# Optimization experiments

Measured on AMD Instinct MI355X. Metric: run time of the kernel, lower is better.

Reference implementation:

```python
import jax, jax.numpy as jnp
import numpy as np

B, C, H, W = 2, 128, 64, 256
G, P, EXP = 8, 4, 2
D = C // G


def _conv1x1(x, w, b):
    # x: (b,c,h,w), w: (o,c), b: (o,)
    return jnp.einsum('bchw,oc->bohw', x, w) + b[None, :, None, None]


def _lin_sample(value, x):
    # value: (b,g,d,h,w); x: (b,g,p,h,w) pixel coords along W -> (b,g,d,p,h,w)
    Bv, Gv, Dv, Hv, Wv = value.shape
    Pv = x.shape[2]
    xc = jnp.clip(x, 0.0, Wv - 1.0)
    x0 = jnp.floor(xc)
    i0 = x0.astype(jnp.int32)
    i1 = jnp.minimum(i0 + 1, Wv - 1)
    t = (xc - x0)[:, :, None]  # (b,g,1,p,h,w)
    shape = (Bv, Gv, Dv, Pv, Hv, Wv)
    v = jnp.broadcast_to(value[:, :, :, None], shape)
    v0 = jnp.take_along_axis(v, jnp.broadcast_to(i0[:, :, None], shape), axis=-1)
    v1 = jnp.take_along_axis(v, jnp.broadcast_to(i1[:, :, None], shape), axis=-1)
    return v0 * (1.0 - t) + v1 * t


def _layernorm_c(x, g, b):
    mu = jnp.mean(x, axis=1, keepdims=True)
    var = jnp.mean((x - mu) ** 2, axis=1, keepdims=True)
    return (x - mu) * jax.lax.rsqrt(var + 1e-5) * g[None, :, None, None] + b[None, :, None, None]


def _forward(ml, mr, fl, fr, nl, nr, gml, gmr, cap, gap,
             wv, bv, wn, bn, woc, boc, wog, bog, wa, ba, wo, bo,
             lw, lb, w1, b1, w2, b2):
    mask = jnp.concatenate([gml, gmr], axis=0)   # (2B,1,H,W)
    q = jnp.concatenate([ml, mr], axis=0)        # (2B,C,H,W)
    ctx = jnp.concatenate([fr, fl], axis=0)      # cross: right feats for left queries
    geo = jnp.concatenate([nr, nl], axis=0)      # (2B,3,H,W)
    B2 = q.shape[0]
    # deformable 1D cross-attention (normal-guided)
    value = _conv1x1(ctx, wv, bv).reshape(B2, G, D, H, W)
    nfeat = _conv1x1(geo, wn, bn).reshape(B2, G, D, H, W)
    off_c = _conv1x1(q, woc, boc).reshape(B2, G, P, H, W)
    off_g = _conv1x1(q, wog, bog).reshape(B2, G, P, H, W)
    attn = jax.nn.softmax(_conv1x1(q, wa, ba).reshape(B2, G, 2 * P, H, W), axis=2)
    ctx_kp = jnp.clip(cap * (W - 1.0) + off_c, 0.0, W - 1.0)
    geo_kp = jnp.clip(gap * (W - 1.0) + off_g, 0.0, W - 1.0)
    s_ctx = _lin_sample(value, ctx_kp)           # (2B,G,D,P,H,W)
    s_geo = _lin_sample(nfeat, geo_kp)
    sampled = jnp.concatenate([s_ctx, s_geo], axis=3)  # (2B,G,D,2P,H,W)
    agg = jnp.einsum('bgdphw,bgphw->bgdhw', sampled, attn).reshape(B2, C, H, W)
    upd = _conv1x1(agg, wo, bo) * mask
    # residual + LayerNorm over channels + 1x1-conv FFN
    x = q + upd
    x = _layernorm_c(x, lw, lb)
    h1 = _conv1x1(x, w1, b1)
    x = x + _conv1x1(h1 * jax.nn.sigmoid(h1), w2, b2)
    return x, ctx_kp, geo_kp


def setup_inputs() -> dict:
    key = jax.random.key(0)
    ks = jax.random.split(key, 20)
    f32 = jnp.float32
    def n(k, shape, s=1.0):
        return jax.random.normal(k, shape, dtype=f32) * s
    return {
        'match_left': n(ks[0], (B, C, H, W)),
        'match_right': n(ks[1], (B, C, H, W)),
        'feat_left': n(ks[2], (B, C, H, W)),
        'feat_right': n(ks[3], (B, C, H, W)),
        'normal_left': n(ks[4], (B, 3, H, W)),
        'normal_right': n(ks[5], (B, 3, H, W)),
        'gate_mask_left': jax.random.uniform(ks[6], (B, 1, H, W), dtype=f32),
        'gate_mask_right': jax.random.uniform(ks[7], (B, 1, H, W), dtype=f32),
        'context_anchor_points': jax.random.uniform(ks[8], (2 * B, G, P, H, W), dtype=f32),
        'geometric_anchor_points': jax.random.uniform(ks[9], (2 * B, G, P, H, W), dtype=f32),
        'w_value': n(ks[10], (C, C), 0.02), 'b_value': jnp.zeros((C,), f32),
        'w_normal': n(ks[11], (C, 3), 0.02), 'b_normal': jnp.zeros((C,), f32),
        'w_off_ctx': n(ks[12], (G * P, C), 0.02), 'b_off_ctx': jnp.zeros((G * P,), f32),
        'w_off_geo': n(ks[13], (G * P, C), 0.02), 'b_off_geo': jnp.zeros((G * P,), f32),
        'w_attn': n(ks[14], (G * 2 * P, C), 0.02), 'b_attn': jnp.zeros((G * 2 * P,), f32),
        'w_out': n(ks[15], (C, C), 0.02), 'b_out': jnp.zeros((C,), f32),
        'ln_w': jnp.ones((C,), f32), 'ln_b': jnp.zeros((C,), f32),
        'w_ff1': n(ks[16], (EXP * C, C), 0.02), 'b_ff1': jnp.zeros((EXP * C,), f32),
        'w_ff2': n(ks[17], (C, EXP * C), 0.02), 'b_ff2': jnp.zeros((C,), f32),
    }


def reference(match_left, match_right, feat_left, feat_right, normal_left, normal_right,
              gate_mask_left, gate_mask_right, context_anchor_points, geometric_anchor_points,
              w_value, b_value, w_normal, b_normal, w_off_ctx, b_off_ctx, w_off_geo, b_off_geo,
              w_attn, b_attn, w_out, b_out, ln_w, ln_b, w_ff1, b_ff1, w_ff2, b_ff2):
    x, ckp, gkp = _forward(match_left, match_right, feat_left, feat_right, normal_left, normal_right,
                           gate_mask_left, gate_mask_right, context_anchor_points, geometric_anchor_points,
                           w_value, b_value, w_normal, b_normal, w_off_ctx, b_off_ctx, w_off_geo, b_off_geo,
                           w_attn, b_attn, w_out, b_out, ln_w, ln_b, w_ff1, b_ff1, w_ff2, b_ff2)
    ml, mr = jnp.split(x, 2, axis=0)
    return (ml, mr, ckp, gkp)
```

## Files before the change

### kernel.cpp

```cpp
#include <hip/hip_runtime.h>
#include <cstdint>
#include <math.h>

#define B2v 4
#define Cc  128
#define Hh  64
#define Ww  256
#define Gg  8
#define Pp  4
#define HW  (Hh*Ww)
#define CHW (Cc*HW)
#define PIT 136

typedef float f32x4 __attribute__((ext_vector_type(4)));
typedef float f32x2 __attribute__((ext_vector_type(2)));
typedef short s16x8 __attribute__((ext_vector_type(8)));
typedef short s16x4 __attribute__((ext_vector_type(4)));

__device__ __forceinline__ short f2bf(float x) {
    union { float f; unsigned u; } a; a.f = x;
    unsigned r = a.u + 0x7fffu + ((a.u >> 16) & 1u);
    return (short)(r >> 16);
}
__device__ __forceinline__ float bf2f(short s) {
    union { unsigned u; float f; } a; a.u = ((unsigned)(unsigned short)s) << 16;
    return a.f;
}
__device__ __forceinline__ unsigned cvtpk(float lo, float hi) {
    unsigned r;
    asm("v_cvt_pk_bf16_f32 %0, %1, %2" : "=v"(r) : "v"(lo), "v"(hi));
    return r;
}
__device__ __forceinline__ f32x2 unpk(unsigned w) {
    union { unsigned u; float f; } lo, hi;
    lo.u = w << 16; hi.u = w & 0xffff0000u;
    return (f32x2){lo.f, hi.f};
}
__device__ __forceinline__ float frcp(float x) { return __builtin_amdgcn_rcpf(x); }
__device__ __forceinline__ float fexp(float x) { return __expf(x); }

__global__ __launch_bounds__(256) void prep_kernel(
    const float* __restrict__ wv, const float* __restrict__ woc,
    const float* __restrict__ wog, const float* __restrict__ wa,
    const float* __restrict__ wo, const float* __restrict__ w1,
    const float* __restrict__ w2,
    const float* __restrict__ boc, const float* __restrict__ bog,
    const float* __restrict__ ba,
    short* __restrict__ wbf, float* __restrict__ bq)
{
    int i = blockIdx.x * 256 + threadIdx.x;
    if (i < 16384) wbf[i] = f2bf(wv[i]);
    else if (i < 32768) {
        int j = i - 16384; int r = j >> 7, c = j & 127;
        float v = (r < 32) ? woc[r * 128 + c] : (r < 64) ? wog[(r - 32) * 128 + c]
                                              : wa[(r - 64) * 128 + c];
        wbf[i] = f2bf(v);
    }
    else if (i < 49152)  wbf[i] = f2bf(wo[i - 32768]);
    else if (i < 81920)  wbf[i] = f2bf(w1[i - 49152]);
    else if (i < 114688) wbf[i] = f2bf(w2[i - 81920]);
    else if (i < 114816) {
        int r = i - 114688;
        bq[r] = (r < 32) ? boc[r] : (r < 64) ? bog[r - 32] : ba[r - 64];
    }
}

__global__ __launch_bounds__(1024, 4) void mega_kernel(
    const float* __restrict__ mlq, const float* __restrict__ mrq,
    const float* __restrict__ fl,  const float* __restrict__ fr,
    const float* __restrict__ nl,  const float* __restrict__ nr,
    const float* __restrict__ gml, const float* __restrict__ gmr,
    const float* __restrict__ cap, const float* __restrict__ gap,
    const short* __restrict__ wbf, const float* __restrict__ bq,
    const float* __restrict__ bv,
    const float* __restrict__ wn,  const float* __restrict__ bn,
    const float* __restrict__ bo,
    const float* __restrict__ lnw, const float* __restrict__ lnb,
    const float* __restrict__ b1,  const float* __restrict__ b2,
    float* __restrict__ out_ml, float* __restrict__ out_mr,
    float* __restrict__ ckp_out, float* __restrict__ gkp_out)
{
    __shared__ short buf1[256 * PIT];
    __shared__ short buf2[256 * PIT];
    __shared__ f32x4 sgeo4[256];
    __shared__ f32x2 swnp[256];
    __shared__ float sln[256];
    __shared__ float redS[1024], redQ[1024];
    __shared__ float smu[256], srs[256];

    const short* wv_bf = wbf;
    const short* wq_bf = wbf + 16384;
    const short* wo_bf = wbf + 32768;
    const short* w1_bf = wbf + 49152;
    const short* w2_bf = wbf + 81920;

    const int t    = threadIdx.x;
    const int lane = t & 63;
    const int wvid = t >> 6;
    const int rw   = wvid & 7;
    const int pw   = wvid >> 3;
    const int lm   = lane & 15;
    const int lq   = lane >> 4;
    const int h = blockIdx.x, b = blockIdx.y;
    const int hWw = h * Ww;
    const int px   = t & 255;
    const int qt   = t >> 8;

    const float* ctx = (b < 2) ? fr + (size_t)b * CHW : fl + (size_t)(b - 2) * CHW;
    const float* q   = (b < 2) ? mlq + (size_t)b * CHW : mrq + (size_t)(b - 2) * CHW;
    const float* geo = (b < 2) ? nr + (size_t)b * 3 * HW : nl + (size_t)(b - 2) * 3 * HW;
    const float* msk = (b < 2) ? gml + (size_t)b * HW : gmr + (size_t)(b - 2) * HW;
    float* outp = (b < 2) ? out_ml + (size_t)b * CHW : out_mr + (size_t)(b - 2) * CHW;

    float capr[8], gapr[8];
    const size_t kbase = ((size_t)b * Gg + qt * 2) * Pp * (size_t)HW + hWw + px;
    {
#pragma unroll
        for (int i = 0; i < 8; i++) {
            capr[i] = cap[kbase + (size_t)i * HW];
            gapr[i] = gap[kbase + (size_t)i * HW];
        }
    }

    if (t < 256) {
        sgeo4[t] = (f32x4){geo[hWw + t], geo[HW + hWw + t], geo[2 * HW + hWw + t], 0.f};
        const int pr = t >> 2, m = t & 3;
        const int ch0 = pr * 2, ch1 = ch0 + 1;
        float a0 = (m < 3) ? wn[ch0 * 3 + m] : bn[ch0];
        float a1 = (m < 3) ? wn[ch1 * 3 + m] : bn[ch1];
        swnp[t] = (f32x2){a0, a1};
    }
    else if (t < 512) {
        int i = t - 256;
        sln[i] = (i < 128) ? lnw[i] : lnb[i - 128];
    }

    {
        const int c0 = wvid * 8;
        const int p0 = lane * 4;
        const size_t gbase = (size_t)c0 * HW + hWw + p0;
        {
            f32x4 L[8];
#pragma unroll
            for (int c = 0; c < 8; c++) L[c] = *(const f32x4*)(ctx + gbase + (size_t)c * HW);
#pragma unroll
            for (int j = 0; j < 4; j++) {
                uint4 w0;
                w0.x = cvtpk(L[0][j], L[1][j]);  w0.y = cvtpk(L[2][j], L[3][j]);
                w0.z = cvtpk(L[4][j], L[5][j]);  w0.w = cvtpk(L[6][j], L[7][j]);
                *(uint4*)(&buf1[(p0 + j) * PIT + c0]) = w0;
            }
        }
        {
            f32x4 L[8];
#pragma unroll
            for (int c = 0; c < 8; c++) L[c] = *(const f32x4*)(q + gbase + (size_t)c * HW);
#pragma unroll
            for (int j = 0; j < 4; j++) {
                uint4 w0;
                w0.x = cvtpk(L[0][j], L[1][j]);  w0.y = cvtpk(L[2][j], L[3][j]);
                w0.z = cvtpk(L[4][j], L[5][j]);  w0.w = cvtpk(L[6][j], L[7][j]);
                *(uint4*)(&buf2[(p0 + j) * PIT + c0]) = w0;
            }
        }
    }
    __syncthreads();

    f32x4 accv[8];
#pragma unroll
    for (int nt = 0; nt < 8; nt++) accv[nt] = (f32x4){0.f, 0.f, 0.f, 0.f};
#pragma unroll
    for (int kk = 0; kk < 4; kk++) {
        s16x8 a = *(const s16x8*)(wv_bf + (size_t)(rw * 16 + lm) * 128 + kk * 32 + lq * 8);
#pragma unroll
        for (int nt = 0; nt < 8; nt++) {
            s16x8 bfv = *(const s16x8*)(&buf1[((pw * 8 + nt) * 16 + lm) * PIT + kk * 32 + lq * 8]);
            accv[nt] = __builtin_amdgcn_mfma_f32_16x16x32_bf16(a, bfv, accv[nt], 0, 0, 0);
        }
    }
    __syncthreads();

    {
        const int ob = rw * 16 + lq * 4;
        float bias[4];
#pragma unroll
        for (int r = 0; r < 4; r++) bias[r] = bv[ob + r];
#pragma unroll
        for (int nt = 0; nt < 8; nt++) {
            const int wg = (pw * 8 + nt) * 16 + lm;
            uint2 pk;
            pk.x = cvtpk(accv[nt][0] + bias[0], accv[nt][1] + bias[1]);
            pk.y = cvtpk(accv[nt][2] + bias[2], accv[nt][3] + bias[3]);
            *(uint2*)(&buf1[wg * PIT + ob]) = pk;
        }
    }
    f32x4 accp[8];
#pragma unroll
    for (int nt = 0; nt < 8; nt++) accp[nt] = (f32x4){0.f, 0.f, 0.f, 0.f};
#pragma unroll
    for (int kk = 0; kk < 4; kk++) {
        s16x8 a = *(const s16x8*)(wq_bf + (size_t)(rw * 16 + lm) * 128 + kk * 32 + lq * 8);
#pragma unroll
        for (int nt = 0; nt < 8; nt++) {
            s16x8 bfv = *(const s16x8*)(&buf2[((pw * 8 + nt) * 16 + lm) * PIT + kk * 32 + lq * 8]);
            accp[nt] = __builtin_amdgcn_mfma_f32_16x16x32_bf16(a, bfv, accp[nt], 0, 0, 0);
        }
    }
    __syncthreads();

    {
        const int ob = rw * 16 + lq * 4;
        float bias[4];
#pragma unroll
        for (int r = 0; r < 4; r++) bias[r] = bq[ob + r];
#pragma unroll
        for (int nt = 0; nt < 8; nt++) {
            const int wg = (pw * 8 + nt) * 16 + lm;
            uint2 pk;
            pk.x = cvtpk(accp[nt][0] + bias[0], accp[nt][1] + bias[1]);
            pk.y = cvtpk(accp[nt][2] + bias[2], accp[nt][3] + bias[3]);
            *(uint2*)(&buf2[wg * PIT + ob]) = pk;
        }
    }
    __syncthreads();

    float attnr[2][8], kpr[2][8];
#pragma unroll
    for (int gi = 0; gi < 2; gi++) {
        const int g = qt * 2 + gi;
        s16x8 lg = *(const s16x8*)(&buf2[px * PIT + 64 + g * 8]);
        float L[8], m = -1e30f;
#pragma unroll
        for (int j = 0; j < 8; j++) { L[j] = bf2f(lg[j]); m = fmaxf(m, L[j]); }
        float s = 0.f;
#pragma unroll
        for (int j = 0; j < 8; j++) { L[j] = fexp(L[j] - m); s += L[j]; }
        float inv = frcp(s);
#pragma unroll
        for (int j = 0; j < 8; j++) attnr[gi][j] = L[j] * inv;
#pragma unroll
        for (int p = 0; p < 4; p++) {
            size_t kidx = kbase + (size_t)(gi * 4 + p) * HW;
            float oc = bf2f(buf2[px * PIT + g * 4 + p]);
            float og = bf2f(buf2[px * PIT + 32 + g * 4 + p]);
            float ck = fminf(fmaxf(capr[gi * 4 + p] * 255.0f + oc, 0.f), 255.f);
            float gk = fminf(fmaxf(gapr[gi * 4 + p] * 255.0f + og, 0.f), 255.f);
            ckp_out[kidx] = ck;
            gkp_out[kidx] = gk;
            kpr[gi][p] = ck;
            kpr[gi][4 + p] = gk;
        }
    }
    __syncthreads();

#pragma unroll
    for (int gi = 0; gi < 2; gi++) {
        const int g = qt * 2 + gi;
        f32x2 A[8];
#pragma unroll
        for (int k = 0; k < 8; k++) A[k] = (f32x2){0.f, 0.f};
#pragma unroll
        for (int j = 0; j < 4; j++) {
            float x = kpr[gi][j];
            float fx = floorf(x);
            int i0 = (int)fx;
            int i1 = min(i0 + 1, Ww - 1);
            float tt = x - fx;
            float c0 = attnr[gi][j] * (1.f - tt);
            float c1 = attnr[gi][j] * tt;
            f32x2 c0v = {c0, c0}, c1v = {c1, c1};
            uint4 v0a = *(const uint4*)(&buf1[i0 * PIT + g * 16]);
            uint4 v0b = *(const uint4*)(&buf1[i0 * PIT + g * 16 + 8]);
            uint4 v1a = *(const uint4*)(&buf1[i1 * PIT + g * 16]);
            uint4 v1b = *(const uint4*)(&buf1[i1 * PIT + g * 16 + 8]);
            const unsigned w0[8] = {v0a.x, v0a.y, v0a.z, v0a.w, v0b.x, v0b.y, v0b.z, v0b.w};
            const unsigned w1[8] = {v1a.x, v1a.y, v1a.z, v1a.w, v1b.x, v1b.y, v1b.z, v1b.w};
#pragma unroll
            for (int k = 0; k < 8; k++)
                A[k] += unpk(w0[k]) * c0v + unpk(w1[k]) * c1v;
        }
        {
            float gs0 = 0.f, gs1 = 0.f, gs2 = 0.f, as = 0.f;
#pragma unroll
            for (int j = 4; j < 8; j++) {
                float x = kpr[gi][j];
                float fx = floorf(x);
                int i0 = (int)fx;
                int i1 = min(i0 + 1, Ww - 1);
                float tt = x - fx;
                float c0 = attnr[gi][j] * (1.f - tt);
                float c1 = attnr[gi][j] * tt;
                f32x4 ga = sgeo4[i0], gb = sgeo4[i1];
                gs0 += c0 * ga[0] + c1 * gb[0];
                gs1 += c0 * ga[1] + c1 * gb[1];
                gs2 += c0 * ga[2] + c1 * gb[2];
                as  += attnr[gi][j];
            }
            f32x2 g0v = {gs0, gs0}, g1v = {gs1, gs1}, g2v = {gs2, gs2}, asv = {as, as};
#pragma unroll
            for (int k = 0; k < 8; k++) {
                const f32x2* wp = &swnp[(g * 8 + k) * 4];
                A[k] += wp[0] * g0v + wp[1] * g1v + wp[2] * g2v + wp[3] * asv;
            }
        }
        uint4 o0, o1;
        o0.x = cvtpk(A[0][0], A[0][1]); o0.y = cvtpk(A[1][0], A[1][1]);
        o0.z = cvtpk(A[2][0], A[2][1]); o0.w = cvtpk(A[3][0], A[3][1]);
        o1.x = cvtpk(A[4][0], A[4][1]); o1.y = cvtpk(A[5][0], A[5][1]);
        o1.z = cvtpk(A[6][0], A[6][1]); o1.w = cvtpk(A[7][0], A[7][1]);
        *(uint4*)(&buf2[px * PIT + g * 16])     = o0;
        *(uint4*)(&buf2[px * PIT + g * 16 + 8]) = o1;
    }
    __syncthreads();

    {
        f32x4 acc1[8];
#pragma unroll
        for (int nt = 0; nt < 8; nt++) acc1[nt] = (f32x4){0.f, 0.f, 0.f, 0.f};
#pragma unroll
        for (int kk = 0; kk < 4; kk++) {
            s16x8 a = *(const s16x8*)(wo_bf + (size_t)(rw * 16 + lm) * 128 + kk * 32 + lq * 8);
#pragma unroll
            for (int nt = 0; nt < 8; nt++) {
                s16x8 bfv = *(const s16x8*)(&buf2[((pw * 8 + nt) * 16 + lm) * PIT + kk * 32 + lq * 8]);
                acc1[nt] = __builtin_amdgcn_mfma_f32_16x16x32_bf16(a, bfv, acc1[nt], 0, 0, 0);
            }
        }
        const int ob = rw * 16 + lq * 4;
        float bias[4];
#pragma unroll
        for (int r = 0; r < 4; r++) bias[r] = bo[ob + r];
#pragma unroll
        for (int nt = 0; nt < 8; nt++) {
            const int wg = (pw * 8 + nt) * 16 + lm;
            float mval = msk[hWw + wg];
            float xv[4];
#pragma unroll
            for (int r = 0; r < 4; r++) {
                float upd = acc1[nt][r] + bias[r];
                float qv = q[(size_t)(ob + r) * HW + hWw + wg];
                xv[r] = qv + upd * mval;
            }
            uint2 pk;
            pk.x = cvtpk(xv[0], xv[1]);
            pk.y = cvtpk(xv[2], xv[3]);
            *(uint2*)(&buf1[wg * PIT + ob]) = pk;
        }
    }
    __syncthreads();

    {
        float ls = 0.f, lsq = 0.f;
#pragma unroll
        for (int c8 = 0; c8 < 4; c8++) {
            uint4 u = *(const uint4*)(&buf1[px * PIT + qt * 32 + c8 * 8]);
            const unsigned wv4[4] = {u.x, u.y, u.z, u.w};
#pragma unroll
            for (int j2 = 0; j2 < 4; j2++) {
                f32x2 e = unpk(wv4[j2]);
                ls  += e[0] + e[1];
                lsq += e[0] * e[0] + e[1] * e[1];
            }
        }
        redS[t] = ls; redQ[t] = lsq;
        __syncthreads();
        if (t < 256) {
            float s  = redS[t] + redS[t + 256] + redS[t + 512] + redS[t + 768];
            float qq = redQ[t] + redQ[t + 256] + redQ[t + 512] + redQ[t + 768];
            float mu = s * (1.f / 128.f);
            float var = qq * (1.f / 128.f) - mu * mu;
            smu[t] = mu;
            srs[t] = __builtin_amdgcn_rsqf(var + 1e-5f);
        }
        __syncthreads();
        const float mu = smu[px], rs = srs[px];
#pragma unroll
        for (int c8 = 0; c8 < 4; c8++) {
            const int cb = qt * 32 + c8 * 8;
            uint4 u = *(const uint4*)(&buf1[px * PIT + cb]);
            const unsigned wv4[4] = {u.x, u.y, u.z, u.w};
            uint4 o;
            unsigned res[4];
#pragma unroll
            for (int j2 = 0; j2 < 4; j2++) {
                f32x2 e = unpk(wv4[j2]);
                const int c = cb + j2 * 2;
                float a0 = rs * sln[c],     bb0 = sln[128 + c]     - mu * a0;
                float a1 = rs * sln[c + 1], bb1 = sln[128 + c + 1] - mu * a1;
                res[j2] = cvtpk(e[0] * a0 + bb0, e[1] * a1 + bb1);
            }
            o.x = res[0]; o.y = res[1]; o.z = res[2]; o.w = res[3];
            *(uint4*)(&buf1[px * PIT + cb]) = o;
        }
    }
    __syncthreads();

    f32x4 acc3[8];
#pragma unroll
    for (int nt = 0; nt < 8; nt++) acc3[nt] = (f32x4){0.f, 0.f, 0.f, 0.f};

    for (int jc = 0; jc < 2; jc++) {
        f32x4 acc2[8];
#pragma unroll
        for (int nt = 0; nt < 8; nt++) acc2[nt] = (f32x4){0.f, 0.f, 0.f, 0.f};
#pragma unroll
        for (int kk = 0; kk < 4; kk++) {
            s16x8 a = *(const s16x8*)(w1_bf + (size_t)(jc * 128 + rw * 16 + lm) * 128 + kk * 32 + lq * 8);
#pragma unroll
            for (int nt = 0; nt < 8; nt++) {
                s16x8 bfv = *(const s16x8*)(&buf1[((pw * 8 + nt) * 16 + lm) * PIT + kk * 32 + lq * 8]);
                acc2[nt] = __builtin_amdgcn_mfma_f32_16x16x32_bf16(a, bfv, acc2[nt], 0, 0, 0);
            }
        }
        {
            const int jb = rw * 16 + lq * 4;
            float bias[4];
#pragma unroll
            for (int r = 0; r < 4; r++) bias[r] = b1[jc * 128 + jb + r];
#pragma unroll
            for (int nt = 0; nt < 8; nt++) {
                const int wg = (pw * 8 + nt) * 16 + lm;
                float o[4];
#pragma unroll
                for (int r = 0; r < 4; r++) {
                    float hv = acc2[nt][r] + bias[r];
                    o[r] = hv * frcp(1.f + fexp(-hv));
                }
                uint2 pk;
                pk.x = cvtpk(o[0], o[1]);
                pk.y = cvtpk(o[2], o[3]);
                *(uint2*)(&buf2[wg * PIT + jb]) = pk;
            }
        }
        __syncthreads();
#pragma unroll
        for (int kk = 0; kk < 4; kk++) {
            s16x8 a = *(const s16x8*)(w2_bf + (size_t)(rw * 16 + lm) * 256 + jc * 128 + kk * 32 + lq * 8);
#pragma unroll
            for (int nt = 0; nt < 8; nt++) {
                s16x8 bfv = *(const s16x8*)(&buf2[((pw * 8 + nt) * 16 + lm) * PIT + kk * 32 + lq * 8]);
                acc3[nt] = __builtin_amdgcn_mfma_f32_16x16x32_bf16(a, bfv, acc3[nt], 0, 0, 0);
            }
        }
        __syncthreads();
    }

    {
        const int ob = rw * 16 + lq * 4;
        float b2v[4];
#pragma unroll
        for (int r = 0; r < 4; r++) b2v[r] = b2[ob + r];
#pragma unroll
        for (int nt = 0; nt < 8; nt++) {
            const int wg = (pw * 8 + nt) * 16 + lm;
            s16x4 xn4 = *(const s16x4*)(&buf1[wg * PIT + ob]);
#pragma unroll
            for (int r = 0; r < 4; r++)
                outp[(size_t)(ob + r) * HW + hWw + wg] = bf2f(xn4[r]) + b2v[r] + acc3[nt][r];
        }
    }
}

extern "C" void kernel_launch(void* const* d_in, const int* in_sizes, int n_in,
                              void* d_out, int out_size, void* d_ws, size_t ws_size,
                              hipStream_t stream)
{
    const float* match_l = (const float*)d_in[0];
    const float* match_r = (const float*)d_in[1];
    const float* feat_l  = (const float*)d_in[2];
    const float* feat_r  = (const float*)d_in[3];
    const float* norm_l  = (const float*)d_in[4];
    const float* norm_r  = (const float*)d_in[5];
    const float* gml     = (const float*)d_in[6];
    const float* gmr     = (const float*)d_in[7];
    const float* cap     = (const float*)d_in[8];
    const float* gap     = (const float*)d_in[9];
    const float* wv  = (const float*)d_in[10]; const float* bv  = (const float*)d_in[11];
    const float* wn  = (const float*)d_in[12]; const float* bn  = (const float*)d_in[13];
    const float* woc = (const float*)d_in[14]; const float* boc = (const float*)d_in[15];
    const float* wog = (const float*)d_in[16]; const float* bog = (const float*)d_in[17];
    const float* wa  = (const float*)d_in[18]; const float* ba  = (const float*)d_in[19];
    const float* wo  = (const float*)d_in[20]; const float* bo  = (const float*)d_in[21];
    const float* lnw = (const float*)d_in[22]; const float* lnb = (const float*)d_in[23];
    const float* w1  = (const float*)d_in[24]; const float* b1  = (const float*)d_in[25];
    const float* w2  = (const float*)d_in[26]; const float* b2  = (const float*)d_in[27];

    float* out = (float*)d_out;
    float* out_ml  = out;
    float* out_mr  = out + (size_t)2 * CHW;
    float* ckp_out = out + (size_t)4 * CHW;
    float* gkp_out = ckp_out + (size_t)B2v * Gg * Pp * HW;

    float* ws = (float*)d_ws;
    float* bq  = ws;
    short* wbf = (short*)(bq + 128);

    prep_kernel<<<dim3(449), dim3(256), 0, stream>>>(
        wv, woc, wog, wa, wo, w1, w2, boc, bog, ba, wbf, bq);
    mega_kernel<<<dim3(Hh, B2v), dim3(1024), 0, stream>>>(
        match_l, match_r, feat_l, feat_r, norm_l, norm_r, gml, gmr, cap, gap,
        wbf, bq, bv, wn, bn, bo, lnw, lnb, b1, b2,
        out_ml, out_mr, ckp_out, gkp_out);
}
```

Measured before the change: 213.8 us.

## Split value projection into separate kernel and process half-rows in main kernel

Moves the value 1x1 conv into its own kernel that writes bf16 values per row to a global workspace. The main kernel now processes 128-pixel half-rows with 512 threads, halving LDS buffers and doubling the grid, and gathers sampled values from global memory. This aims to raise occupancy and block-level parallelism. In exchange it adds a kernel launch, a global write and reread of the value tensor, and uncached-LDS gathers turn into global loads.

New measurement: 220.6 us. +3.2%, slower.

```diff
diff --git a/kernel.cpp b/kernel.cpp
--- a/kernel.cpp
+++ b/kernel.cpp
@@ -38,6 +38,7 @@
 }
 __device__ __forceinline__ float frcp(float x) { return __builtin_amdgcn_rcpf(x); }
 __device__ __forceinline__ float fexp(float x) { return __expf(x); }
+#define MFMA16(a, bfr, c) __builtin_amdgcn_mfma_f32_16x16x32_bf16((a), (bfr), (c), 0, 0, 0)
 
 __global__ __launch_bounds__(256) void prep_kernel(
     const float* __restrict__ wv, const float* __restrict__ woc,
@@ -65,35 +66,12 @@
     }
 }
 
-__global__ __launch_bounds__(1024, 4) void mega_kernel(
-    const float* __restrict__ mlq, const float* __restrict__ mrq,
-    const float* __restrict__ fl,  const float* __restrict__ fr,
-    const float* __restrict__ nl,  const float* __restrict__ nr,
-    const float* __restrict__ gml, const float* __restrict__ gmr,
-    const float* __restrict__ cap, const float* __restrict__ gap,
-    const short* __restrict__ wbf, const float* __restrict__ bq,
-    const float* __restrict__ bv,
-    const float* __restrict__ wn,  const float* __restrict__ bn,
-    const float* __restrict__ bo,
-    const float* __restrict__ lnw, const float* __restrict__ lnb,
-    const float* __restrict__ b1,  const float* __restrict__ b2,
-    float* __restrict__ out_ml, float* __restrict__ out_mr,
-    float* __restrict__ ckp_out, float* __restrict__ gkp_out)
+__global__ __launch_bounds__(1024, 4) void value_kernel(
+    const float* __restrict__ fl, const float* __restrict__ fr,
+    const short* __restrict__ wbf, const float* __restrict__ bv,
+    short* __restrict__ valg)
 {
-    __shared__ short buf1[256 * PIT];
-    __shared__ short buf2[256 * PIT];
-    __shared__ f32x4 sgeo4[256];
-    __shared__ f32x2 swnp[256];
-    __shared__ float sln[256];
-    __shared__ float redS[1024], redQ[1024];
-    __shared__ float smu[256], srs[256];
-
-    const short* wv_bf = wbf;
-    const short* wq_bf = wbf + 16384;
-    const short* wo_bf = wbf + 32768;
-    const short* w1_bf = wbf + 49152;
-    const short* w2_bf = wbf + 81920;
-
+    __shared__ short buf[256 * PIT];
     const int t    = threadIdx.x;
     const int lane = t & 63;
     const int wvid = t >> 6;
@@ -103,17 +81,117 @@
     const int lq   = lane >> 4;
     const int h = blockIdx.x, b = blockIdx.y;
     const int hWw = h * Ww;
-    const int px   = t & 255;
-    const int qt   = t >> 8;
-
     const float* ctx = (b < 2) ? fr + (size_t)b * CHW : fl + (size_t)(b - 2) * CHW;
+    const short* wv_bf = wbf;
+
+    {
+        const int c0 = wvid * 8;
+        const int p0 = lane * 4;
+        const size_t gbase = (size_t)c0 * HW + hWw + p0;
+        f32x4 L[8];
+#pragma unroll
+        for (int c = 0; c < 8; c++) L[c] = *(const f32x4*)(ctx + gbase + (size_t)c * HW);
+#pragma unroll
+        for (int j = 0; j < 4; j++) {
+            uint4 w0;
+            w0.x = cvtpk(L[0][j], L[1][j]);  w0.y = cvtpk(L[2][j], L[3][j]);
+            w0.z = cvtpk(L[4][j], L[5][j]);  w0.w = cvtpk(L[6][j], L[7][j]);
+            *(uint4*)(&buf[(p0 + j) * PIT + c0]) = w0;
+        }
+    }
+    __syncthreads();
+
+    f32x4 acc[8];
+#pragma unroll
+    for (int nt = 0; nt < 8; nt++) acc[nt] = (f32x4){0.f, 0.f, 0.f, 0.f};
+#pragma unroll
+    for (int kk = 0; kk < 4; kk++) {
+        s16x8 a = *(const s16x8*)(wv_bf + (size_t)(rw * 16 + lm) * 128 + kk * 32 + lq * 8);
+#pragma unroll
+        for (int nt = 0; nt < 8; nt++) {
+            s16x8 bfr = *(const s16x8*)(&buf[((pw * 8 + nt) * 16 + lm) * PIT + kk * 32 + lq * 8]);
+            acc[nt] = MFMA16(a, bfr, acc[nt]);
+        }
+    }
+    __syncthreads();
+
+    {
+        const int ob = rw * 16 + lq * 4;
+        float bias[4];
+#pragma unroll
+        for (int r = 0; r < 4; r++) bias[r] = bv[ob + r];
+#pragma unroll
+        for (int nt = 0; nt < 8; nt++) {
+            const int wg = (pw * 8 + nt) * 16 + lm;
+            uint2 pk;
+            pk.x = cvtpk(acc[nt][0] + bias[0], acc[nt][1] + bias[1]);
+            pk.y = cvtpk(acc[nt][2] + bias[2], acc[nt][3] + bias[3]);
+            *(uint2*)(&buf[wg * PIT + ob]) = pk;
+        }
+    }
+    __syncthreads();
+
+    {
+        short* dst = valg + ((size_t)b * HW + hWw) * 128;
+        for (int i = t; i < 4096; i += 1024) {
+            const int row = i >> 4, seg = i & 15;
+            *(uint4*)(dst + (size_t)row * 128 + seg * 8) =
+                *(const uint4*)(&buf[row * PIT + seg * 8]);
+        }
+    }
+}
+
+__global__ __launch_bounds__(512, 4) void mega_kernel(
+    const float* __restrict__ mlq, const float* __restrict__ mrq,
+    const float* __restrict__ nl,  const float* __restrict__ nr,
+    const float* __restrict__ gml, const float* __restrict__ gmr,
+    const float* __restrict__ cap, const float* __restrict__ gap,
+    const short* __restrict__ wbf, const float* __restrict__ bq,
+    const short* __restrict__ valg,
+    const float* __restrict__ wn,  const float* __restrict__ bn,
+    const float* __restrict__ bo,
+    const float* __restrict__ lnw, const float* __restrict__ lnb,
+    const float* __restrict__ b1,  const float* __restrict__ b2,
+    float* __restrict__ out_ml, float* __restrict__ out_mr,
+    float* __restrict__ ckp_out, float* __restrict__ gkp_out)
+{
+    __shared__ short buf1[128 * PIT];
+    __shared__ short buf2[128 * PIT];
+    __shared__ f32x4 sgeo4[256];
+    __shared__ f32x2 swnp[256];
+    __shared__ float sln[256];
+
+    float* redS = (float*)buf2;
+    float* redQ = redS + 512;
+    float* smu  = redQ + 512;
+    float* srs  = smu + 128;
+
+    const short* wq_bf = wbf + 16384;
+    const short* wo_bf = wbf + 32768;
+    const short* w1_bf = wbf + 49152;
+    const short* w2_bf = wbf + 81920;
+
+    const int t    = threadIdx.x;
+    const int lane = t & 63;
+    const int ww   = t >> 6;
+    const int lm   = lane & 15;
+    const int lq   = lane >> 4;
+    const int hh = blockIdx.x, b = blockIdx.y;
+    const int h = hh >> 1;
+    const int pxb = (hh & 1) * 128;
+    const int hWw = h * Ww;
+    const int rowoff = hWw + pxb;
+    const int pxl  = t & 127;
+    const int qt   = t >> 7;
+
     const float* q   = (b < 2) ? mlq + (size_t)b * CHW : mrq + (size_t)(b - 2) * CHW;
     const float* geo = (b < 2) ? nr + (size_t)b * 3 * HW : nl + (size_t)(b - 2) * 3 * HW;
     const float* msk = (b < 2) ? gml + (size_t)b * HW : gmr + (size_t)(b - 2) * HW;
     float* outp = (b < 2) ? out_ml + (size_t)b * CHW : out_mr + (size_t)(b - 2) * CHW;
+    const short* valrow = valg + ((size_t)b * HW + hWw) * 128;
 
     float capr[8], gapr[8];
-    const size_t kbase = ((size_t)b * Gg + qt * 2) * Pp * (size_t)HW + hWw + px;
+    const size_t kbase = ((size_t)b * Gg + qt * 2) * Pp * (size_t)HW + rowoff + pxl;
     {
 #pragma unroll
         for (int i = 0; i < 8; i++) {
@@ -124,102 +202,58 @@
 
     if (t < 256) {
         sgeo4[t] = (f32x4){geo[hWw + t], geo[HW + hWw + t], geo[2 * HW + hWw + t], 0.f};
-        const int pr = t >> 2, m = t & 3;
+        sln[t] = (t < 128) ? lnw[t] : lnb[t - 128];
+    } else {
+        const int i = t - 256;
+        const int pr = i >> 2, m = i & 3;
         const int ch0 = pr * 2, ch1 = ch0 + 1;
         float a0 = (m < 3) ? wn[ch0 * 3 + m] : bn[ch0];
         float a1 = (m < 3) ? wn[ch1 * 3 + m] : bn[ch1];
-        swnp[t] = (f32x2){a0, a1};
-    }
-    else if (t < 512) {
-        int i = t - 256;
-        sln[i] = (i < 128) ? lnw[i] : lnb[i - 128];
-    }
-
-    {
-        const int c0 = wvid * 8;
-        const int p0 = lane * 4;
-        const size_t gbase = (size_t)c0 * HW + hWw + p0;
-        {
-            f32x4 L[8];
-#pragma unroll
-            for (int c = 0; c < 8; c++) L[c] = *(const f32x4*)(ctx + gbase + (size_t)c * HW);
-#pragma unroll
-            for (int j = 0; j < 4; j++) {
-                uint4 w0;
-                w0.x = cvtpk(L[0][j], L[1][j]);  w0.y = cvtpk(L[2][j], L[3][j]);
-                w0.z = cvtpk(L[4][j], L[5][j]);  w0.w = cvtpk(L[6][j], L[7][j]);
-                *(uint4*)(&buf1[(p0 + j) * PIT + c0]) = w0;
-            }
-        }
-        {
-            f32x4 L[8];
-#pragma unroll
-            for (int c = 0; c < 8; c++) L[c] = *(const f32x4*)(q + gbase + (size_t)c * HW);
-#pragma unroll
-            for (int j = 0; j < 4; j++) {
-                uint4 w0;
-                w0.x = cvtpk(L[0][j], L[1][j]);  w0.y = cvtpk(L[2][j], L[3][j]);
-                w0.z = cvtpk(L[4][j], L[5][j]);  w0.w = cvtpk(L[6][j], L[7][j]);
-                *(uint4*)(&buf2[(p0 + j) * PIT + c0]) = w0;
-            }
-        }
-    }
-    __syncthreads();
-
-    f32x4 accv[8];
-#pragma unroll
-    for (int nt = 0; nt < 8; nt++) accv[nt] = (f32x4){0.f, 0.f, 0.f, 0.f};
-#pragma unroll
-    for (int kk = 0; kk < 4; kk++) {
-        s16x8 a = *(const s16x8*)(wv_bf + (size_t)(rw * 16 + lm) * 128 + kk * 32 + lq * 8);
+        swnp[i] = (f32x2){a0, a1};
+    }
+
+    {
+        const int c0 = ww * 16 + (lane >> 5) * 8;
+        const int p0 = (lane & 31) * 4;
+        const size_t gbase = (size_t)c0 * HW + rowoff + p0;
+        f32x4 L[8];
+#pragma unroll
+        for (int c = 0; c < 8; c++) L[c] = *(const f32x4*)(q + gbase + (size_t)c * HW);
+#pragma unroll
+        for (int j = 0; j < 4; j++) {
+            uint4 w0;
+            w0.x = cvtpk(L[0][j], L[1][j]);  w0.y = cvtpk(L[2][j], L[3][j]);
+            w0.z = cvtpk(L[4][j], L[5][j]);  w0.w = cvtpk(L[6][j], L[7][j]);
+            *(uint4*)(&buf1[(p0 + j) * PIT + c0]) = w0;
+        }
+    }
+    __syncthreads();
+
+    {
+        f32x4 accp[8];
+#pragma unroll
+        for (int nt = 0; nt < 8; nt++) accp[nt] = (f32x4){0.f, 0.f, 0.f, 0.f};
+#pragma unroll
+        for (int kk = 0; kk < 4; kk++) {
+            s16x8 a = *(const s16x8*)(wq_bf + (size_t)(ww * 16 + lm) * 128 + kk * 32 + lq * 8);
+#pragma unroll
+            for (int nt = 0; nt < 8; nt++) {
+                s16x8 bfr = *(const s16x8*)(&buf1[(nt * 16 + lm) * PIT + kk * 32 + lq * 8]);
+                accp[nt] = MFMA16(a, bfr, accp[nt]);
+            }
+        }
+        __syncthreads();
+        const int ob = ww * 16 + lq * 4;
+        float bias[4];
+#pragma unroll
+        for (int r = 0; r < 4; r++) bias[r] = bq[ob + r];
 #pragma unroll
         for (int nt = 0; nt < 8; nt++) {
-            s16x8 bfv = *(const s16x8*)(&buf1[((pw * 8 + nt) * 16 + lm) * PIT + kk * 32 + lq * 8]);
-            accv[nt] = __builtin_amdgcn_mfma_f32_16x16x32_bf16(a, bfv, accv[nt], 0, 0, 0);
-        }
-    }
-    __syncthreads();
-
-    {
-        const int ob = rw * 16 + lq * 4;
-        float bias[4];
-#pragma unroll
-        for (int r = 0; r < 4; r++) bias[r] = bv[ob + r];
-#pragma unroll
-        for (int nt = 0; nt < 8; nt++) {
-            const int wg = (pw * 8 + nt) * 16 + lm;
-            uint2 pk;
-            pk.x = cvtpk(accv[nt][0] + bias[0], accv[nt][1] + bias[1]);
-            pk.y = cvtpk(accv[nt][2] + bias[2], accv[nt][3] + bias[3]);
-            *(uint2*)(&buf1[wg * PIT + ob]) = pk;
-        }
-    }
-    f32x4 accp[8];
-#pragma unroll
-    for (int nt = 0; nt < 8; nt++) accp[nt] = (f32x4){0.f, 0.f, 0.f, 0.f};
-#pragma unroll
-    for (int kk = 0; kk < 4; kk++) {
-        s16x8 a = *(const s16x8*)(wq_bf + (size_t)(rw * 16 + lm) * 128 + kk * 32 + lq * 8);
-#pragma unroll
-        for (int nt = 0; nt < 8; nt++) {
-            s16x8 bfv = *(const s16x8*)(&buf2[((pw * 8 + nt) * 16 + lm) * PIT + kk * 32 + lq * 8]);
-            accp[nt] = __builtin_amdgcn_mfma_f32_16x16x32_bf16(a, bfv, accp[nt], 0, 0, 0);
-        }
-    }
-    __syncthreads();
-
-    {
-        const int ob = rw * 16 + lq * 4;
-        float bias[4];
-#pragma unroll
-        for (int r = 0; r < 4; r++) bias[r] = bq[ob + r];
-#pragma unroll
-        for (int nt = 0; nt < 8; nt++) {
-            const int wg = (pw * 8 + nt) * 16 + lm;
+            const int wg = nt * 16 + lm;
             uint2 pk;
             pk.x = cvtpk(accp[nt][0] + bias[0], accp[nt][1] + bias[1]);
             pk.y = cvtpk(accp[nt][2] + bias[2], accp[nt][3] + bias[3]);
-            *(uint2*)(&buf2[wg * PIT + ob]) = pk;
+            *(uint2*)(&buf1[wg * PIT + ob]) = pk;
         }
     }
     __syncthreads();
@@ -228,7 +262,7 @@
 #pragma unroll
     for (int gi = 0; gi < 2; gi++) {
         const int g = qt * 2 + gi;
-        s16x8 lg = *(const s16x8*)(&buf2[px * PIT + 64 + g * 8]);
+        s16x8 lg = *(const s16x8*)(&buf1[pxl * PIT + 64 + g * 8]);
         float L[8], m = -1e30f;
 #pragma unroll
         for (int j = 0; j < 8; j++) { L[j] = bf2f(lg[j]); m = fmaxf(m, L[j]); }
@@ -241,8 +275,8 @@
 #pragma unroll
         for (int p = 0; p < 4; p++) {
             size_t kidx = kbase + (size_t)(gi * 4 + p) * HW;
-            float oc = bf2f(buf2[px * PIT + g * 4 + p]);
-            float og = bf2f(buf2[px * PIT + 32 + g * 4 + p]);
+            float oc = bf2f(buf1[pxl * PIT + g * 4 + p]);
+            float og = bf2f(buf1[pxl * PIT + 32 + g * 4 + p]);
             float ck = fminf(fmaxf(capr[gi * 4 + p] * 255.0f + oc, 0.f), 255.f);
             float gk = fminf(fmaxf(gapr[gi * 4 + p] * 255.0f + og, 0.f), 255.f);
             ckp_out[kidx] = ck;
@@ -269,10 +303,12 @@
             float c0 = attnr[gi][j] * (1.f - tt);
             float c1 = attnr[gi][j] * tt;
             f32x2 c0v = {c0, c0}, c1v = {c1, c1};
-            uint4 v0a = *(const uint4*)(&buf1[i0 * PIT + g * 16]);
-            uint4 v0b = *(const uint4*)(&buf1[i0 * PIT + g * 16 + 8]);
-            uint4 v1a = *(const uint4*)(&buf1[i1 * PIT + g * 16]);
-            uint4 v1b = *(const uint4*)(&buf1[i1 * PIT + g * 16 + 8]);
+            const short* v0p = valrow + (size_t)i0 * 128 + g * 16;
+            const short* v1p = valrow + (size_t)i1 * 128 + g * 16;
+            uint4 v0a = *(const uint4*)(v0p);
+            uint4 v0b = *(const uint4*)(v0p + 8);
+            uint4 v1a = *(const uint4*)(v1p);
+            uint4 v1b = *(const uint4*)(v1p + 8);
             const unsigned w0[8] = {v0a.x, v0a.y, v0a.z, v0a.w, v0b.x, v0b.y, v0b.z, v0b.w};
             const unsigned w1[8] = {v1a.x, v1a.y, v1a.z, v1a.w, v1b.x, v1b.y, v1b.z, v1b.w};
 #pragma unroll
@@ -308,8 +344,8 @@
         o0.z = cvtpk(A[2][0], A[2][1]); o0.w = cvtpk(A[3][0], A[3][1]);
         o1.x = cvtpk(A[4][0], A[4][1]); o1.y = cvtpk(A[5][0], A[5][1]);
         o1.z = cvtpk(A[6][0], A[6][1]); o1.w = cvtpk(A[7][0], A[7][1]);
-        *(uint4*)(&buf2[px * PIT + g * 16])     = o0;
-        *(uint4*)(&buf2[px * PIT + g * 16 + 8]) = o1;
+        *(uint4*)(&buf1[pxl * PIT + g * 16])     = o0;
+        *(uint4*)(&buf1[pxl * PIT + g * 16 + 8]) = o1;
     }
     __syncthreads();
 
@@ -319,27 +355,27 @@
         for (int nt = 0; nt < 8; nt++) acc1[nt] = (f32x4){0.f, 0.f, 0.f, 0.f};
 #pragma unroll
         for (int kk = 0; kk < 4; kk++) {
-            s16x8 a = *(const s16x8*)(wo_bf + (size_t)(rw * 16 + lm) * 128 + kk * 32 + lq * 8);
+            s16x8 a = *(const s16x8*)(wo_bf + (size_t)(ww * 16 + lm) * 128 + kk * 32 + lq * 8);
 #pragma unroll
             for (int nt = 0; nt < 8; nt++) {
-                s16x8 bfv = *(const s16x8*)(&buf2[((pw * 8 + nt) * 16 + lm) * PIT + kk * 32 + lq * 8]);
-                acc1[nt] = __builtin_amdgcn_mfma_f32_16x16x32_bf16(a, bfv, acc1[nt], 0, 0, 0);
-            }
-        }
-        const int ob = rw * 16 + lq * 4;
+                s16x8 bfr = *(const s16x8*)(&buf1[(nt * 16 + lm) * PIT + kk * 32 + lq * 8]);
+                acc1[nt] = MFMA16(a, bfr, acc1[nt]);
+            }
+        }
+        __syncthreads();
+        const int ob = ww * 16 + lq * 4;
         float bias[4];
 #pragma unroll
         for (int r = 0; r < 4; r++) bias[r] = bo[ob + r];
 #pragma unroll
         for (int nt = 0; nt < 8; nt++) {
-            const int wg = (pw * 8 + nt) * 16 + lm;
-            float mval = msk[hWw + wg];
+            const int wg = nt * 16 + lm;
+            const float mval = msk[rowoff + wg];
             float xv[4];
 #pragma unroll
             for (int r = 0; r < 4; r++) {
-                float upd = acc1[nt][r] + bias[r];
-                float qv = q[(size_t)(ob + r) * HW + hWw + wg];
-                xv[r] = qv + upd * mval;
+                float qv = q[(size_t)(ob + r) * HW + rowoff + wg];
+                xv[r] = qv + (acc1[nt][r] + bias[r]) * mval;
             }
             uint2 pk;
             pk.x = cvtpk(xv[0], xv[1]);
@@ -353,7 +389,7 @@
         float ls = 0.f, lsq = 0.f;
 #pragma unroll
         for (int c8 = 0; c8 < 4; c8++) {
-            uint4 u = *(const uint4*)(&buf1[px * PIT + qt * 32 + c8 * 8]);
+            uint4 u = *(const uint4*)(&buf1[pxl * PIT + qt * 32 + c8 * 8]);
             const unsigned wv4[4] = {u.x, u.y, u.z, u.w};
 #pragma unroll
             for (int j2 = 0; j2 < 4; j2++) {
@@ -364,20 +400,20 @@
         }
         redS[t] = ls; redQ[t] = lsq;
         __syncthreads();
-        if (t < 256) {
-            float s  = redS[t] + redS[t + 256] + redS[t + 512] + redS[t + 768];
-            float qq = redQ[t] + redQ[t + 256] + redQ[t + 512] + redQ[t + 768];
+        if (t < 128) {
+            float s  = redS[t] + redS[t + 128] + redS[t + 256] + redS[t + 384];
+            float qq = redQ[t] + redQ[t + 128] + redQ[t + 256] + redQ[t + 384];
             float mu = s * (1.f / 128.f);
             float var = qq * (1.f / 128.f) - mu * mu;
             smu[t] = mu;
             srs[t] = __builtin_amdgcn_rsqf(var + 1e-5f);
         }
         __syncthreads();
-        const float mu = smu[px], rs = srs[px];
+        const float mu = smu[pxl], rs = srs[pxl];
 #pragma unroll
         for (int c8 = 0; c8 < 4; c8++) {
             const int cb = qt * 32 + c8 * 8;
-            uint4 u = *(const uint4*)(&buf1[px * PIT + cb]);
+            uint4 u = *(const uint4*)(&buf1[pxl * PIT + cb]);
             const unsigned wv4[4] = {u.x, u.y, u.z, u.w};
             uint4 o;
             unsigned res[4];
@@ -390,7 +426,7 @@
                 res[j2] = cvtpk(e[0] * a0 + bb0, e[1] * a1 + bb1);
             }
             o.x = res[0]; o.y = res[1]; o.z = res[2]; o.w = res[3];
-            *(uint4*)(&buf1[px * PIT + cb]) = o;
+            *(uint4*)(&buf1[pxl * PIT + cb]) = o;
         }
     }
     __syncthreads();
@@ -405,21 +441,21 @@
         for (int nt = 0; nt < 8; nt++) acc2[nt] = (f32x4){0.f, 0.f, 0.f, 0.f};
 #pragma unroll
         for (int kk = 0; kk < 4; kk++) {
-            s16x8 a = *(const s16x8*)(w1_bf + (size_t)(jc * 128 + rw * 16 + lm) * 128 + kk * 32 + lq * 8);
+            s16x8 a = *(const s16x8*)(w1_bf + (size_t)(jc * 128 + ww * 16 + lm) * 128 + kk * 32 + lq * 8);
 #pragma unroll
             for (int nt = 0; nt < 8; nt++) {
-                s16x8 bfv = *(const s16x8*)(&buf1[((pw * 8 + nt) * 16 + lm) * PIT + kk * 32 + lq * 8]);
-                acc2[nt] = __builtin_amdgcn_mfma_f32_16x16x32_bf16(a, bfv, acc2[nt], 0, 0, 0);
+                s16x8 bfr = *(const s16x8*)(&buf1[(nt * 16 + lm) * PIT + kk * 32 + lq * 8]);
+                acc2[nt] = MFMA16(a, bfr, acc2[nt]);
             }
         }
         {
-            const int jb = rw * 16 + lq * 4;
+            const int jb = ww * 16 + lq * 4;
             float bias[4];
 #pragma unroll
             for (int r = 0; r < 4; r++) bias[r] = b1[jc * 128 + jb + r];
 #pragma unroll
             for (int nt = 0; nt < 8; nt++) {
-                const int wg = (pw * 8 + nt) * 16 + lm;
+                const int wg = nt * 16 + lm;
                 float o[4];
 #pragma unroll
                 for (int r = 0; r < 4; r++) {
@@ -435,28 +471,29 @@
         __syncthreads();
 #pragma unroll
         for (int kk = 0; kk < 4; kk++) {
-            s16x8 a = *(const s16x8*)(w2_bf + (size_t)(rw * 16 + lm) * 256 + jc * 128 + kk * 32 + lq * 8);
+            s16x8 a = *(const s16x8*)(w2_bf + (size_t)(ww * 16 + lm) * 256 + jc * 128 + kk * 32 + lq * 8);
 #pragma unroll
             for (int nt = 0; nt < 8; nt++) {
-                s16x8 bfv = *(const s16x8*)(&buf2[((pw * 8 + nt) * 16 + lm) * PIT + kk * 32 + lq * 8]);
-                acc3[nt] = __builtin_amdgcn_mfma_f32_16x16x32_bf16(a, bfv, acc3[nt], 0, 0, 0);
+                s16x8 bfr = *(const s16x8*)(&buf2[(nt * 16 + lm) * PIT + kk * 32 + lq * 8]);
+                acc3[nt] = MFMA16(a, bfr, acc3[nt]);
             }
         }
         __syncthreads();
     }
 
     {
-        const int ob = rw * 16 + lq * 4;
+        const int ob = ww * 16 + lq * 4;
         float b2v[4];
 #pragma unroll
         for (int r = 0; r < 4; r++) b2v[r] = b2[ob + r];
 #pragma unroll
         for (int nt = 0; nt < 8; nt++) {
-            const int wg = (pw * 8 + nt) * 16 + lm;
+            const int wg = nt * 16 + lm;
             s16x4 xn4 = *(const s16x4*)(&buf1[wg * PIT + ob]);
 #pragma unroll
             for (int r = 0; r < 4; r++)
-                outp[(size_t)(ob + r) * HW + hWw + wg] = bf2f(xn4[r]) + b2v[r] + acc3[nt][r];
+                outp[(size_t)(ob + r) * HW + rowoff + wg] =
+                    bf2f(xn4[r]) + b2v[r] + acc3[nt][r];
         }
     }
 }
@@ -494,11 +531,14 @@
     float* ws = (float*)d_ws;
     float* bq  = ws;
     short* wbf = (short*)(bq + 128);
+    short* valg = wbf + 114688;
 
     prep_kernel<<<dim3(449), dim3(256), 0, stream>>>(
         wv, woc, wog, wa, wo, w1, w2, boc, bog, ba, wbf, bq);
-    mega_kernel<<<dim3(Hh, B2v), dim3(1024), 0, stream>>>(
-        match_l, match_r, feat_l, feat_r, norm_l, norm_r, gml, gmr, cap, gap,
-        wbf, bq, bv, wn, bn, bo, lnw, lnb, b1, b2,
+    value_kernel<<<dim3(Hh, B2v), dim3(1024), 0, stream>>>(
+        feat_l, feat_r, wbf, bv, valg);
+    mega_kernel<<<dim3(Hh * 2, B2v), dim3(512), 0, stream>>>(
+        match_l, match_r, norm_l, norm_r, gml, gmr, cap, gap,
+        wbf, bq, valg, wn, bn, bo, lnw, lnb, b1, b2,
         out_ml, out_mr, ckp_out, gkp_out);
 }
```
